# Optimization experiments

Hardware: AMD Instinct MI355X
Metric: run time of the kernel (lower is better)

Reference implementation:

```python
import jax, jax.numpy as jnp
import numpy as np
import math


def _conv1x1(x, w, b):
    # x: [B,C,H,W], w: [O,C], b: [O] -> [B,O,H,W]
    return jnp.einsum('oc,bchw->bohw', w, x) + b[None, :, None, None]


def _attn_branch(x, f_w, f_b, g_w, g_b, h_w, h_b, gamma):
    B, C, H, W = x.shape
    N = H * W
    k_dim = C // 8
    f = _conv1x1(x, f_w, f_b).reshape(B, k_dim, N)  # [B,k,N]
    g = _conv1x1(x, g_w, g_b).reshape(B, k_dim, N)  # [B,k,N]
    # attention[b, n, m] = sum_k f[b,k,n] * g[b,k,m] / sqrt(k_dim)
    scores = jnp.einsum('bkn,bkm->bnm', f, g) / math.sqrt(k_dim)
    attn = jax.nn.softmax(scores, axis=2)  # softmax over last dim (dim=2)
    h = _conv1x1(x, h_w, h_b).reshape(B, C, N)  # [B,C,N]
    sa_map = jnp.einsum('bcn,bnm->bcm', h, attn).reshape(B, C, H, W)
    return gamma[0] * sa_map + x


def setup_inputs() -> dict:
    key = jax.random.key(0)
    ks = jax.random.split(key, 8)
    B, C, H, W = 4, 256, 64, 64
    kd = C // 8
    scale_in = 1.0 / math.sqrt(C)
    return {
        'x1': jax.random.normal(ks[0], (B, C, H, W), jnp.float32),
        'x2': jax.random.normal(ks[1], (B, C, H, W), jnp.float32),
        'f_w': jax.random.normal(ks[2], (kd, C), jnp.float32) * scale_in,
        'f_b': jnp.zeros((kd,), jnp.float32),
        'g_w': jax.random.normal(ks[3], (kd, C), jnp.float32) * scale_in,
        'g_b': jnp.zeros((kd,), jnp.float32),
        'h1_w': jax.random.normal(ks[4], (C, C), jnp.float32) * scale_in,
        'h1_b': jnp.zeros((C,), jnp.float32),
        'h2_w': jax.random.normal(ks[5], (C, C), jnp.float32) * scale_in,
        'h2_b': jnp.zeros((C,), jnp.float32),
        'gamma1': jax.random.normal(ks[6], (1,), jnp.float32),
        'gamma2': jax.random.normal(ks[7], (1,), jnp.float32),
    }


def reference(x1, x2, f_w, f_b, g_w, g_b, h1_w, h1_b, h2_w, h2_b, gamma1, gamma2):
    y1 = _attn_branch(x1, f_w, f_b, g_w, g_b, h1_w, h1_b, gamma1)
    y2 = _attn_branch(x2, f_w, f_b, g_w, g_b, h2_w, h2_b, gamma2)
    return (y1, y2)
```

## Files before the change

### kernel.cpp

```cpp
#include <hip/hip_runtime.h>
#include <hip/hip_bf16.h>
#include <math.h>

#define NDIM 4096
#define CDIM 256
#define KD   32
#define SCALE 0.17677669529663687f
#define ALPHA (0.17677669529663687f * 1.44269504088896341f)
#define SHIFT2 11.541560327111707f

typedef __attribute__((ext_vector_type(8))) short short8;
typedef __attribute__((ext_vector_type(4))) float f32x4;
typedef unsigned short u16;
typedef unsigned int u32;

__device__ __forceinline__ u32 f2bf(float x) {
  union { float f; u32 u; } v; v.f = x;
  return (v.u + 0x7FFFu + ((v.u >> 16) & 1u)) >> 16;
}

__device__ __forceinline__ u32 pack_bf16x2(float a, float b) {
  __hip_bfloat162 h2 = __float22bfloat162_rn(make_float2(a, b));
  u32 r;
  __builtin_memcpy(&r, &h2, 4);
  return r;
}

#define MFMA16(a, b, c) __builtin_amdgcn_mfma_f32_16x16x32_bf16((a), (b), (c), 0, 0, 0)

__global__ void cast_all_kernel(const float* __restrict__ h1w,
                                const float* __restrict__ h2w,
                                const float* __restrict__ fw,
                                const float* __restrict__ gw,
                                u16* __restrict__ dst) {
  int i = blockIdx.x * 256 + threadIdx.x;
  float v;
  if (i < 65536) v = h1w[i];
  else if (i < 131072) v = h2w[i - 65536];
  else if (i < 139264) v = fw[i - 131072] * ALPHA;
  else v = gw[i - 139264];
  dst[i] = (u16)f2bf(v);
}

__global__ __launch_bounds__(256) void transpose_cast_kernel(
    const float* __restrict__ x1, const float* __restrict__ x2,
    u16* __restrict__ xt) {
  __shared__ float ts[64][68];
  const int t = threadIdx.x;
  const int ntile = blockIdx.x * 64, Ctile = blockIdx.y * 64, z = blockIdx.z;
  const float* xb = ((z >> 2) ? x2 : x1) + (size_t)(z & 3) * CDIM * NDIM;
  u16* xtb = xt + (size_t)z * NDIM * CDIM;
  const int r = t >> 4, c4 = (t & 15) * 4;
#pragma unroll
  for (int i = 0; i < 4; i++) {
    float4 v = *(const float4*)&xb[(size_t)(Ctile + r + i * 16) * NDIM + ntile + c4];
    *(float4*)&ts[r + i * 16][c4] = v;
  }
  __syncthreads();
  const int n = t >> 2, Cg = (t & 3) * 16;
  u32 pk[8];
#pragma unroll
  for (int j = 0; j < 8; j++) {
    u32 lo = f2bf(ts[Cg + 2 * j][n]);
    u32 hi = f2bf(ts[Cg + 2 * j + 1][n]);
    pk[j] = lo | (hi << 16);
  }
  uint4* dst = (uint4*)&xtb[(size_t)(ntile + n) * CDIM + Ctile + Cg];
  dst[0] = make_uint4(pk[0], pk[1], pk[2], pk[3]);
  dst[1] = make_uint4(pk[4], pk[5], pk[6], pk[7]);
}

__global__ __launch_bounds__(256) void conv_fg_kernel(
    const u16* __restrict__ Wf, const float* __restrict__ fbias,
    const u16* __restrict__ Wg, const float* __restrict__ gbias,
    const u16* __restrict__ xt, u16* __restrict__ ftT, u16* __restrict__ gtT) {
  const int t = threadIdx.x, w = t >> 6, l = t & 63, li = l & 15, q = l >> 4;
  const int ntile = blockIdx.x * 64, bb = blockIdx.y;
  const u16* xtb = xt + (size_t)bb * NDIM * CDIM;
  f32x4 zero4 = {0.f, 0.f, 0.f, 0.f};
  f32x4 acc[2][2];
  for (int i = 0; i < 2; i++) for (int j = 0; j < 2; j++) acc[i][j] = zero4;
  const int nrow = ntile + w * 16 + li;

  for (int k0 = 0; k0 < CDIM; k0 += 32) {
    short8 bx = *(const short8*)&xtb[(size_t)nrow * CDIM + k0 + q * 8];
    short8 af0 = *(const short8*)&Wf[(size_t)(li) * CDIM + k0 + q * 8];
    short8 af1 = *(const short8*)&Wf[(size_t)(16 + li) * CDIM + k0 + q * 8];
    short8 ag0 = *(const short8*)&Wg[(size_t)(li) * CDIM + k0 + q * 8];
    short8 ag1 = *(const short8*)&Wg[(size_t)(16 + li) * CDIM + k0 + q * 8];
    acc[0][0] = MFMA16(af0, bx, acc[0][0]);
    acc[0][1] = MFMA16(af1, bx, acc[0][1]);
    acc[1][0] = MFMA16(ag0, bx, acc[1][0]);
    acc[1][1] = MFMA16(ag1, bx, acc[1][1]);
  }
  u16* outs[2] = {ftT + (size_t)bb * NDIM * KD, gtT + (size_t)bb * NDIM * KD};
  const float* biases[2] = {fbias, gbias};
  const float bscale[2] = {ALPHA, 1.0f};
#pragma unroll
  for (int fg = 0; fg < 2; fg++) {
#pragma unroll
    for (int os = 0; os < 2; os++) {
      float b0 = biases[fg][os * 16 + q * 4 + 0] * bscale[fg];
      float b1 = biases[fg][os * 16 + q * 4 + 1] * bscale[fg];
      float b2 = biases[fg][os * 16 + q * 4 + 2] * bscale[fg];
      float b3 = biases[fg][os * 16 + q * 4 + 3] * bscale[fg];
      u32 p0 = f2bf(acc[fg][os][0] + b0) | (f2bf(acc[fg][os][1] + b1) << 16);
      u32 p1 = f2bf(acc[fg][os][2] + b2) | (f2bf(acc[fg][os][3] + b3) << 16);
      *(uint2*)&outs[fg][(size_t)nrow * KD + os * 16 + q * 4] = make_uint2(p0, p1);
    }
  }
}

__global__ __launch_bounds__(256) void stats_kernel(
    const u16* __restrict__ ft, const u16* __restrict__ gt,
    float* __restrict__ L) {
  __shared__ float zred[32][64];
  const int t = threadIdx.x, w = t >> 6, l = t & 63, li = l & 15, q = l >> 4;
  const int n0 = blockIdx.x * 32;
  const int bb = blockIdx.z * 4 + blockIdx.y;
  const u16* ftb = ft + (size_t)bb * NDIM * KD;
  const u16* gtb = gt + (size_t)bb * NDIM * KD;
  f32x4 zero4 = {0.f, 0.f, 0.f, 0.f};

  short8 a0 = *(const short8*)&ftb[(size_t)(n0 + li) * KD + q * 8];
  short8 a1 = *(const short8*)&ftb[(size_t)(n0 + 16 + li) * KD + q * 8];
  f32x4 z0 = zero4, z1 = zero4;

#pragma unroll 2
  for (int it = 0; it < 64; it++) {
    int m = (it * 4 + w) * 16;
    short8 bf = *(const short8*)&gtb[(size_t)(m + li) * KD + q * 8];
    f32x4 S0 = MFMA16(a0, bf, zero4);
    f32x4 S1 = MFMA16(a1, bf, zero4);
#pragma unroll
    for (int reg = 0; reg < 4; reg++) {
      z0[reg] += exp2f(S0[reg] - SHIFT2);
      z1[reg] += exp2f(S1[reg] - SHIFT2);
    }
  }
#pragma unroll
  for (int reg = 0; reg < 4; reg++) {
    zred[q * 4 + reg][w * 16 + li] = z0[reg];
    zred[16 + q * 4 + reg][w * 16 + li] = z1[reg];
  }
  __syncthreads();
  const int r = t >> 3, i8 = t & 7;
  float4 s1 = *(const float4*)&zred[r][i8 * 8];
  float4 s2 = *(const float4*)&zred[r][i8 * 8 + 4];
  float sum = s1.x + s1.y + s1.z + s1.w + s2.x + s2.y + s2.z + s2.w;
  sum += __shfl_xor(sum, 1, 8);
  sum += __shfl_xor(sum, 2, 8);
  sum += __shfl_xor(sum, 4, 8);
  if (i8 == 0) L[(size_t)bb * NDIM + n0 + r] = SHIFT2 + __log2f(sum);
}

__global__ __launch_bounds__(256) void conv_h_kernel(
    const u16* __restrict__ Wall, const float* __restrict__ b1,
    const float* __restrict__ b2, const u16* __restrict__ xt,
    const float* __restrict__ L, u16* __restrict__ outH) {
  const int t = threadIdx.x, w = t >> 6, l = t & 63, li = l & 15, q = l >> 4;
  const int ntile = blockIdx.x * 64;
  const int o0 = blockIdx.y * 64 + w * 16;
  const int bb = blockIdx.z, branch = bb >> 2;
  const u16* W = Wall + (size_t)branch * CDIM * CDIM;
  const float* bias = branch ? b2 : b1;
  const u16* xtb = xt + (size_t)bb * NDIM * CDIM;
  const float* Lb = L + (size_t)bb * NDIM;
  u16* ob = outH + (size_t)bb * CDIM * NDIM;
  f32x4 zero4 = {0.f, 0.f, 0.f, 0.f};
  f32x4 acc[4];
  for (int i = 0; i < 4; i++) acc[i] = zero4;

  for (int k0 = 0; k0 < CDIM; k0 += 32) {
    short8 a = *(const short8*)&W[(size_t)(o0 + li) * CDIM + k0 + q * 8];
#pragma unroll
    for (int ns = 0; ns < 4; ns++) {
      short8 bf = *(const short8*)&xtb[(size_t)(ntile + ns * 16 + li) * CDIM + k0 + q * 8];
      acc[ns] = MFMA16(a, bf, acc[ns]);
    }
  }
  float bv[4];
#pragma unroll
  for (int reg = 0; reg < 4; reg++) bv[reg] = bias[o0 + q * 4 + reg];
#pragma unroll
  for (int ns = 0; ns < 4; ns++) {
    int n = ntile + ns * 16 + li;
    float ex = exp2f(-Lb[n]);
#pragma unroll
    for (int reg = 0; reg < 4; reg++) {
      int c = o0 + q * 4 + reg;
      ob[(size_t)c * NDIM + n] = (u16)f2bf((acc[ns][reg] + bv[reg]) * ex);
    }
  }
}

__global__ __launch_bounds__(1024, 4) void apply_kernel(
    const u16* __restrict__ ft, const u16* __restrict__ gt,
    const u16* __restrict__ h,
    const float* __restrict__ x1, const float* __restrict__ x2,
    const float* __restrict__ gamma1, const float* __restrict__ gamma2,
    float* __restrict__ out) {
  __shared__ u16 Pt[2][128][132];
  const int t = threadIdx.x, w = t >> 6, l = t & 63, li = l & 15, q = l >> 4;
  const int bid = blockIdx.x;
  const int bb = bid & 7;
  const int mtile = (bid >> 3) * 128;
  const int br = bb >> 2, b = bb & 3;
  const u16* ftb = ft + (size_t)bb * NDIM * KD;
  const u16* gtb = gt + (size_t)bb * NDIM * KD;
  const u16* hb = h + (size_t)bb * CDIM * NDIM;
  const float* xb = (br ? x2 : x1) + (size_t)b * CDIM * NDIM;
  const float gmv = br ? gamma2[0] : gamma1[0];
  float* ob = out + (size_t)bb * CDIM * NDIM;

  const bool producer = (w & 1) == 0;
  const int pidx = w >> 1;
  const int c0 = (w >> 1) * 32;
  f32x4 zero4 = {0.f, 0.f, 0.f, 0.f};

  short8 gfrag;
  if (producer)
    gfrag = *(const short8*)&gtb[(size_t)(mtile + pidx * 16 + li) * KD + q * 8];

  f32x4 acc[8][2];
#pragma unroll
  for (int i = 0; i < 8; i++)
#pragma unroll
    for (int j = 0; j < 2; j++) acc[i][j] = zero4;

  for (int i = 0; i <= 32; i++) {
    if (producer) {
      if (i < 32) {
        const int n0 = i * 128, buf = i & 1;
        short8 af[8];
#pragma unroll
        for (int j = 0; j < 8; j++)
          af[j] = *(const short8*)&ftb[(size_t)(n0 + j * 16 + li) * KD + q * 8];
#pragma unroll
        for (int j = 0; j < 8; j++) {
          f32x4 S = MFMA16(af[j], gfrag, zero4);
          u32 p0 = pack_bf16x2(exp2f(S[0]), exp2f(S[1]));
          u32 p1 = pack_bf16x2(exp2f(S[2]), exp2f(S[3]));
          *(uint2*)&Pt[buf][pidx * 16 + li][j * 16 + q * 4] = make_uint2(p0, p1);
        }
      }
    } else {
      if (i >= 1) {
        const int n0 = (i - 1) * 128, buf = (i - 1) & 1;
        short8 ah[2][2];
#pragma unroll
        for (int cs = 0; cs < 2; cs++)
          ah[0][cs] = *(const short8*)
              &hb[(size_t)(c0 + cs * 16 + li) * NDIM + n0 + q * 8];
        __builtin_amdgcn_s_setprio(1);
#pragma unroll
        for (int kh = 0; kh < 4; kh++) {
          if (kh < 3) {
#pragma unroll
            for (int cs = 0; cs < 2; cs++)
              ah[(kh + 1) & 1][cs] = *(const short8*)
                  &hb[(size_t)(c0 + cs * 16 + li) * NDIM + n0 + (kh + 1) * 32 + q * 8];
          }
#pragma unroll
          for (int half = 0; half < 2; half++) {
            short8 bm[4];
#pragma unroll
            for (int mi = 0; mi < 4; mi++) {
              const int ms = half * 4 + mi;
              bm[mi] = *(const short8*)&Pt[buf][ms * 16 + li][kh * 32 + q * 8];
            }
            __builtin_amdgcn_sched_barrier(0);
#pragma unroll
            for (int mi = 0; mi < 4; mi++) {
              const int ms = half * 4 + mi;
              acc[ms][0] = MFMA16(bm[mi], ah[kh & 1][0], acc[ms][0]);
              acc[ms][1] = MFMA16(bm[mi], ah[kh & 1][1], acc[ms][1]);
            }
          }
        }
        __builtin_amdgcn_s_setprio(0);
      }
    }
    asm volatile("s_waitcnt lgkmcnt(0)" ::: "memory");
    __builtin_amdgcn_s_barrier();
  }

  if (!producer) {
#pragma unroll
    for (int ms = 0; ms < 8; ms++) {
#pragma unroll
      for (int cs = 0; cs < 2; cs++) {
        int c = c0 + cs * 16 + li;
        int m = mtile + ms * 16 + q * 4;
        size_t idx = (size_t)c * NDIM + m;
        float4 xv = *(const float4*)&xb[idx];
        float4 o;
        o.x = gmv * acc[ms][cs][0] + xv.x;
        o.y = gmv * acc[ms][cs][1] + xv.y;
        o.z = gmv * acc[ms][cs][2] + xv.z;
        o.w = gmv * acc[ms][cs][3] + xv.w;
        *(float4*)&ob[idx] = o;
      }
    }
  }
}

extern "C" void kernel_launch(void* const* d_in, const int* in_sizes, int n_in,
                              void* d_out, int out_size, void* d_ws, size_t ws_size,
                              hipStream_t stream) {
  const float* x1 = (const float*)d_in[0];
  const float* x2 = (const float*)d_in[1];
  const float* f_w = (const float*)d_in[2];
  const float* f_b = (const float*)d_in[3];
  const float* g_w = (const float*)d_in[4];
  const float* g_b = (const float*)d_in[5];
  const float* h1_w = (const float*)d_in[6];
  const float* h1_b = (const float*)d_in[7];
  const float* h2_w = (const float*)d_in[8];
  const float* h2_b = (const float*)d_in[9];
  const float* gamma1 = (const float*)d_in[10];
  const float* gamma2 = (const float*)d_in[11];
  float* out = (float*)d_out;

  char* ws = (char*)d_ws;
  u16* xt  = (u16*)(ws);
  u16* wh  = (u16*)(ws + 16777216);
  u16* ftw = (u16*)(ws + 33554432);
  u16* gtw = (u16*)(ws + 35651584);
  u16* wWh = (u16*)(ws + 37748736);
  u16* wWf = (u16*)(ws + 38010880);
  u16* wWg = (u16*)(ws + 38027264);
  float* Lw = (float*)(ws + 38043648);

  cast_all_kernel<<<576, 256, 0, stream>>>(h1_w, h2_w, f_w, g_w, wWh);

  transpose_cast_kernel<<<dim3(64, 4, 8), 256, 0, stream>>>(x1, x2, xt);

  conv_fg_kernel<<<dim3(64, 8), 256, 0, stream>>>(wWf, f_b, wWg, g_b, xt, ftw, gtw);

  stats_kernel<<<dim3(128, 4, 2), 256, 0, stream>>>(ftw, gtw, Lw);

  conv_h_kernel<<<dim3(64, 4, 8), 256, 0, stream>>>(wWh, h1_b, h2_b, xt, Lw, wh);

  apply_kernel<<<256, 1024, 0, stream>>>(ftw, gtw, wh, x1, x2,
                                         gamma1, gamma2, out);
}
```

Before: 312.5 us.

## Fuse weight casting, transpose and conv kernels; merge softmax stats with h-conv

Removes the separate weight-cast kernel by converting fp32 weights to bf16 on the fly inside the conv kernels. Fuses the transpose/cast of x with the f/g 1x1 conv, so one block handles all channel tiles of a 64-column strip. Merges the softmax row-statistics kernel with the h conv, keeping the log-sum in shared memory instead of a global buffer. This cuts launches and intermediate traffic, but repeats the weight loads and conversions in every block and gives each fused block more serial work.

```diff
diff --git a/kernel.cpp b/kernel.cpp
--- a/kernel.cpp
+++ b/kernel.cpp
@@ -26,57 +26,62 @@
   return r;
 }
 
+__device__ __forceinline__ short8 load_w8(const float* __restrict__ p,
+                                          float scale) {
+  float4 v0 = *(const float4*)p;
+  float4 v1 = *(const float4*)(p + 4);
+  short8 r;
+  r[0] = (short)f2bf(v0.x * scale);
+  r[1] = (short)f2bf(v0.y * scale);
+  r[2] = (short)f2bf(v0.z * scale);
+  r[3] = (short)f2bf(v0.w * scale);
+  r[4] = (short)f2bf(v1.x * scale);
+  r[5] = (short)f2bf(v1.y * scale);
+  r[6] = (short)f2bf(v1.z * scale);
+  r[7] = (short)f2bf(v1.w * scale);
+  return r;
+}
+
 #define MFMA16(a, b, c) __builtin_amdgcn_mfma_f32_16x16x32_bf16((a), (b), (c), 0, 0, 0)
 
-__global__ void cast_all_kernel(const float* __restrict__ h1w,
-                                const float* __restrict__ h2w,
-                                const float* __restrict__ fw,
-                                const float* __restrict__ gw,
-                                u16* __restrict__ dst) {
-  int i = blockIdx.x * 256 + threadIdx.x;
-  float v;
-  if (i < 65536) v = h1w[i];
-  else if (i < 131072) v = h2w[i - 65536];
-  else if (i < 139264) v = fw[i - 131072] * ALPHA;
-  else v = gw[i - 139264];
-  dst[i] = (u16)f2bf(v);
-}
-
-__global__ __launch_bounds__(256) void transpose_cast_kernel(
+__global__ __launch_bounds__(256) void tfg_kernel(
     const float* __restrict__ x1, const float* __restrict__ x2,
-    u16* __restrict__ xt) {
+    const float* __restrict__ fw, const float* __restrict__ fbias,
+    const float* __restrict__ gw, const float* __restrict__ gbias,
+    u16* __restrict__ xt, u16* __restrict__ ftT, u16* __restrict__ gtT) {
   __shared__ float ts[64][68];
   const int t = threadIdx.x;
-  const int ntile = blockIdx.x * 64, Ctile = blockIdx.y * 64, z = blockIdx.z;
-  const float* xb = ((z >> 2) ? x2 : x1) + (size_t)(z & 3) * CDIM * NDIM;
-  u16* xtb = xt + (size_t)z * NDIM * CDIM;
+  const int bid = blockIdx.x;
+  const int bb = bid & 7;
+  const int ntile = (bid >> 3) * 64;
+  const float* xb = ((bb >> 2) ? x2 : x1) + (size_t)(bb & 3) * CDIM * NDIM;
+  u16* xtb = xt + (size_t)bb * NDIM * CDIM;
+
   const int r = t >> 4, c4 = (t & 15) * 4;
-#pragma unroll
-  for (int i = 0; i < 4; i++) {
-    float4 v = *(const float4*)&xb[(size_t)(Ctile + r + i * 16) * NDIM + ntile + c4];
-    *(float4*)&ts[r + i * 16][c4] = v;
-  }
-  __syncthreads();
   const int n = t >> 2, Cg = (t & 3) * 16;
-  u32 pk[8];
-#pragma unroll
-  for (int j = 0; j < 8; j++) {
-    u32 lo = f2bf(ts[Cg + 2 * j][n]);
-    u32 hi = f2bf(ts[Cg + 2 * j + 1][n]);
-    pk[j] = lo | (hi << 16);
-  }
-  uint4* dst = (uint4*)&xtb[(size_t)(ntile + n) * CDIM + Ctile + Cg];
-  dst[0] = make_uint4(pk[0], pk[1], pk[2], pk[3]);
-  dst[1] = make_uint4(pk[4], pk[5], pk[6], pk[7]);
-}
-
-__global__ __launch_bounds__(256) void conv_fg_kernel(
-    const u16* __restrict__ Wf, const float* __restrict__ fbias,
-    const u16* __restrict__ Wg, const float* __restrict__ gbias,
-    const u16* __restrict__ xt, u16* __restrict__ ftT, u16* __restrict__ gtT) {
-  const int t = threadIdx.x, w = t >> 6, l = t & 63, li = l & 15, q = l >> 4;
-  const int ntile = blockIdx.x * 64, bb = blockIdx.y;
-  const u16* xtb = xt + (size_t)bb * NDIM * CDIM;
+#pragma unroll
+  for (int ct = 0; ct < 4; ct++) {
+    const int Ctile = ct * 64;
+#pragma unroll
+    for (int i = 0; i < 4; i++) {
+      float4 v = *(const float4*)&xb[(size_t)(Ctile + r + i * 16) * NDIM + ntile + c4];
+      *(float4*)&ts[r + i * 16][c4] = v;
+    }
+    __syncthreads();
+    u32 pk[8];
+#pragma unroll
+    for (int j = 0; j < 8; j++) {
+      u32 lo = f2bf(ts[Cg + 2 * j][n]);
+      u32 hi = f2bf(ts[Cg + 2 * j + 1][n]);
+      pk[j] = lo | (hi << 16);
+    }
+    uint4* dst = (uint4*)&xtb[(size_t)(ntile + n) * CDIM + Ctile + Cg];
+    dst[0] = make_uint4(pk[0], pk[1], pk[2], pk[3]);
+    dst[1] = make_uint4(pk[4], pk[5], pk[6], pk[7]);
+    __syncthreads();
+  }
+
+  const int w = t >> 6, l = t & 63, li = l & 15, q = l >> 4;
   f32x4 zero4 = {0.f, 0.f, 0.f, 0.f};
   f32x4 acc[2][2];
   for (int i = 0; i < 2; i++) for (int j = 0; j < 2; j++) acc[i][j] = zero4;
@@ -84,10 +89,10 @@
 
   for (int k0 = 0; k0 < CDIM; k0 += 32) {
     short8 bx = *(const short8*)&xtb[(size_t)nrow * CDIM + k0 + q * 8];
-    short8 af0 = *(const short8*)&Wf[(size_t)(li) * CDIM + k0 + q * 8];
-    short8 af1 = *(const short8*)&Wf[(size_t)(16 + li) * CDIM + k0 + q * 8];
-    short8 ag0 = *(const short8*)&Wg[(size_t)(li) * CDIM + k0 + q * 8];
-    short8 ag1 = *(const short8*)&Wg[(size_t)(16 + li) * CDIM + k0 + q * 8];
+    short8 af0 = load_w8(&fw[(size_t)(li) * CDIM + k0 + q * 8], ALPHA);
+    short8 af1 = load_w8(&fw[(size_t)(16 + li) * CDIM + k0 + q * 8], ALPHA);
+    short8 ag0 = load_w8(&gw[(size_t)(li) * CDIM + k0 + q * 8], 1.0f);
+    short8 ag1 = load_w8(&gw[(size_t)(16 + li) * CDIM + k0 + q * 8], 1.0f);
     acc[0][0] = MFMA16(af0, bx, acc[0][0]);
     acc[0][1] = MFMA16(af1, bx, acc[0][1]);
     acc[1][0] = MFMA16(ag0, bx, acc[1][0]);
@@ -111,21 +116,29 @@
   }
 }
 
-__global__ __launch_bounds__(256) void stats_kernel(
+__global__ __launch_bounds__(256, 4) void sh_kernel(
     const u16* __restrict__ ft, const u16* __restrict__ gt,
-    float* __restrict__ L) {
+    const float* __restrict__ h1w, const float* __restrict__ h2w,
+    const float* __restrict__ b1, const float* __restrict__ b2,
+    const u16* __restrict__ xt, u16* __restrict__ outH) {
   __shared__ float zred[32][64];
+  __shared__ float Lsh[32];
   const int t = threadIdx.x, w = t >> 6, l = t & 63, li = l & 15, q = l >> 4;
-  const int n0 = blockIdx.x * 32;
-  const int bb = blockIdx.z * 4 + blockIdx.y;
+  const int bid = blockIdx.x;
+  const int bb = bid & 7;
+  const int ntile = (bid >> 3) * 32;
+  const int branch = bb >> 2;
   const u16* ftb = ft + (size_t)bb * NDIM * KD;
   const u16* gtb = gt + (size_t)bb * NDIM * KD;
+  const float* Wb = branch ? h2w : h1w;
+  const float* bias = branch ? b2 : b1;
+  const u16* xtb = xt + (size_t)bb * NDIM * CDIM;
+  u16* ob = outH + (size_t)bb * CDIM * NDIM;
   f32x4 zero4 = {0.f, 0.f, 0.f, 0.f};
 
-  short8 a0 = *(const short8*)&ftb[(size_t)(n0 + li) * KD + q * 8];
-  short8 a1 = *(const short8*)&ftb[(size_t)(n0 + 16 + li) * KD + q * 8];
+  short8 a0 = *(const short8*)&ftb[(size_t)(ntile + li) * KD + q * 8];
+  short8 a1 = *(const short8*)&ftb[(size_t)(ntile + 16 + li) * KD + q * 8];
   f32x4 z0 = zero4, z1 = zero4;
-
 #pragma unroll 2
   for (int it = 0; it < 64; it++) {
     int m = (it * 4 + w) * 16;
@@ -144,52 +157,58 @@
     zred[16 + q * 4 + reg][w * 16 + li] = z1[reg];
   }
   __syncthreads();
-  const int r = t >> 3, i8 = t & 7;
-  float4 s1 = *(const float4*)&zred[r][i8 * 8];
-  float4 s2 = *(const float4*)&zred[r][i8 * 8 + 4];
-  float sum = s1.x + s1.y + s1.z + s1.w + s2.x + s2.y + s2.z + s2.w;
-  sum += __shfl_xor(sum, 1, 8);
-  sum += __shfl_xor(sum, 2, 8);
-  sum += __shfl_xor(sum, 4, 8);
-  if (i8 == 0) L[(size_t)bb * NDIM + n0 + r] = SHIFT2 + __log2f(sum);
-}
-
-__global__ __launch_bounds__(256) void conv_h_kernel(
-    const u16* __restrict__ Wall, const float* __restrict__ b1,
-    const float* __restrict__ b2, const u16* __restrict__ xt,
-    const float* __restrict__ L, u16* __restrict__ outH) {
-  const int t = threadIdx.x, w = t >> 6, l = t & 63, li = l & 15, q = l >> 4;
-  const int ntile = blockIdx.x * 64;
-  const int o0 = blockIdx.y * 64 + w * 16;
-  const int bb = blockIdx.z, branch = bb >> 2;
-  const u16* W = Wall + (size_t)branch * CDIM * CDIM;
-  const float* bias = branch ? b2 : b1;
-  const u16* xtb = xt + (size_t)bb * NDIM * CDIM;
-  const float* Lb = L + (size_t)bb * NDIM;
-  u16* ob = outH + (size_t)bb * CDIM * NDIM;
-  f32x4 zero4 = {0.f, 0.f, 0.f, 0.f};
-  f32x4 acc[4];
-  for (int i = 0; i < 4; i++) acc[i] = zero4;
+  {
+    const int rr = t >> 3, i8 = t & 7;
+    float4 s1 = *(const float4*)&zred[rr][i8 * 8];
+    float4 s2 = *(const float4*)&zred[rr][i8 * 8 + 4];
+    float sum = s1.x + s1.y + s1.z + s1.w + s2.x + s2.y + s2.z + s2.w;
+    sum += __shfl_xor(sum, 1, 8);
+    sum += __shfl_xor(sum, 2, 8);
+    sum += __shfl_xor(sum, 4, 8);
+    if (i8 == 0) Lsh[rr] = SHIFT2 + __log2f(sum);
+  }
+  __syncthreads();
+
+  const int o0 = w * 64;
+  f32x4 acch[4][2];
+#pragma unroll
+  for (int i = 0; i < 4; i++)
+#pragma unroll
+    for (int j = 0; j < 2; j++) acch[i][j] = zero4;
 
   for (int k0 = 0; k0 < CDIM; k0 += 32) {
-    short8 a = *(const short8*)&W[(size_t)(o0 + li) * CDIM + k0 + q * 8];
-#pragma unroll
-    for (int ns = 0; ns < 4; ns++) {
-      short8 bf = *(const short8*)&xtb[(size_t)(ntile + ns * 16 + li) * CDIM + k0 + q * 8];
-      acc[ns] = MFMA16(a, bf, acc[ns]);
-    }
-  }
-  float bv[4];
-#pragma unroll
-  for (int reg = 0; reg < 4; reg++) bv[reg] = bias[o0 + q * 4 + reg];
-#pragma unroll
-  for (int ns = 0; ns < 4; ns++) {
-    int n = ntile + ns * 16 + li;
-    float ex = exp2f(-Lb[n]);
-#pragma unroll
-    for (int reg = 0; reg < 4; reg++) {
-      int c = o0 + q * 4 + reg;
-      ob[(size_t)c * NDIM + n] = (u16)f2bf((acc[ns][reg] + bv[reg]) * ex);
+    short8 aw[4];
+#pragma unroll
+    for (int os = 0; os < 4; os++)
+      aw[os] = load_w8(&Wb[(size_t)(o0 + os * 16 + li) * CDIM + k0 + q * 8], 1.0f);
+    short8 bx[2];
+#pragma unroll
+    for (int ns = 0; ns < 2; ns++)
+      bx[ns] = *(const short8*)&xtb[(size_t)(ntile + ns * 16 + li) * CDIM + k0 + q * 8];
+#pragma unroll
+    for (int os = 0; os < 4; os++) {
+      acch[os][0] = MFMA16(aw[os], bx[0], acch[os][0]);
+      acch[os][1] = MFMA16(aw[os], bx[1], acch[os][1]);
+    }
+  }
+  float bv[4][4];
+#pragma unroll
+  for (int os = 0; os < 4; os++)
+#pragma unroll
+    for (int reg = 0; reg < 4; reg++)
+      bv[os][reg] = bias[o0 + os * 16 + q * 4 + reg];
+#pragma unroll
+  for (int ns = 0; ns < 2; ns++) {
+    const int nloc = ns * 16 + li;
+    const int nn = ntile + nloc;
+    const float ex = exp2f(-Lsh[nloc]);
+#pragma unroll
+    for (int os = 0; os < 4; os++) {
+#pragma unroll
+      for (int reg = 0; reg < 4; reg++) {
+        int c = o0 + os * 16 + q * 4 + reg;
+        ob[(size_t)c * NDIM + nn] = (u16)f2bf((acch[os][ns][reg] + bv[os][reg]) * ex);
+      }
     }
   }
 }
@@ -327,20 +346,12 @@
   u16* wh  = (u16*)(ws + 16777216);
   u16* ftw = (u16*)(ws + 33554432);
   u16* gtw = (u16*)(ws + 35651584);
-  u16* wWh = (u16*)(ws + 37748736);
-  u16* wWf = (u16*)(ws + 38010880);
-  u16* wWg = (u16*)(ws + 38027264);
-  float* Lw = (float*)(ws + 38043648);
-
-  cast_all_kernel<<<576, 256, 0, stream>>>(h1_w, h2_w, f_w, g_w, wWh);
-
-  transpose_cast_kernel<<<dim3(64, 4, 8), 256, 0, stream>>>(x1, x2, xt);
-
-  conv_fg_kernel<<<dim3(64, 8), 256, 0, stream>>>(wWf, f_b, wWg, g_b, xt, ftw, gtw);
-
-  stats_kernel<<<dim3(128, 4, 2), 256, 0, stream>>>(ftw, gtw, Lw);
-
-  conv_h_kernel<<<dim3(64, 4, 8), 256, 0, stream>>>(wWh, h1_b, h2_b, xt, Lw, wh);
+
+  tfg_kernel<<<512, 256, 0, stream>>>(x1, x2, f_w, f_b, g_w, g_b,
+                                      xt, ftw, gtw);
+
+  sh_kernel<<<1024, 256, 0, stream>>>(ftw, gtw, h1_w, h2_w, h1_b, h2_b,
+                                      xt, wh);
 
   apply_kernel<<<256, 1024, 0, stream>>>(ftw, gtw, wh, x1, x2,
                                          gamma1, gamma2, out);
```

Measured after the change: 301.3 us. -3.6%, faster.
